# Kernel optimization log

Measured on AMD Instinct MI355X. Metric: run time of the kernel, lower is better.

Reference implementation:

```python
import jax, jax.numpy as jnp
import numpy as np

DIM = 128
HEADS = 4
GH, GW = 14, 14
N = GH * GW            # 196
POS_DIM = (DIM // 4) // 4  # 8, per DynamicPosBias(dim//4): pos_dim = (dim//4)//4
B_ = 1024
NW = 64
EPS = 1e-5


def _make_bias_tables():
    # biases: all relative (dh, dw) offsets, shape ((2*GH-1)*(2*GW-1), 2)
    h = np.arange(1 - GH, GH)
    w = np.arange(1 - GW, GW)
    bh, bw = np.meshgrid(h, w, indexing='ij')
    biases = np.stack([bh.ravel(), bw.ravel()], axis=1).astype(np.float32)
    # relative_position_index: (N, N) int
    ch, cw = np.meshgrid(np.arange(GH), np.arange(GW), indexing='ij')
    coords = np.stack([ch.ravel(), cw.ravel()])          # (2, N)
    rel = coords[:, :, None] - coords[:, None, :]        # (2, N, N)
    rel = rel.transpose(1, 2, 0).copy()
    rel[:, :, 0] += GH - 1
    rel[:, :, 1] += GW - 1
    rel[:, :, 0] *= 2 * GW - 1
    idx = rel.sum(-1).astype(np.int32)                   # (N, N)
    return jnp.asarray(biases), jnp.asarray(idx)


def setup_inputs() -> dict:
    key = jax.random.key(0)
    ks = jax.random.split(key, 12)
    s_in = 1.0 / np.sqrt(DIM)
    s_p = 1.0 / np.sqrt(POS_DIM)
    biases, rel_idx = _make_bias_tables()
    return {
        'x': jax.random.normal(ks[0], (B_, N, DIM), jnp.float32),
        'mask': jnp.zeros((NW, N, N), jnp.float32),
        # qkv / proj (stored as (in, out), i.e. torch weight transposed)
        'qkv_w': jax.random.normal(ks[1], (DIM, 3 * DIM), jnp.float32) * s_in,
        'qkv_b': jnp.zeros((3 * DIM,), jnp.float32),
        'proj_w': jax.random.normal(ks[2], (DIM, DIM), jnp.float32) * s_in,
        'proj_b': jnp.zeros((DIM,), jnp.float32),
        # DynamicPosBias params
        'pos_proj_w': jax.random.normal(ks[3], (2, POS_DIM), jnp.float32) * 0.5,
        'pos_proj_b': jnp.zeros((POS_DIM,), jnp.float32),
        'ln1_w': jnp.ones((POS_DIM,), jnp.float32), 'ln1_b': jnp.zeros((POS_DIM,), jnp.float32),
        'fc1_w': jax.random.normal(ks[4], (POS_DIM, POS_DIM), jnp.float32) * s_p,
        'fc1_b': jnp.zeros((POS_DIM,), jnp.float32),
        'ln2_w': jnp.ones((POS_DIM,), jnp.float32), 'ln2_b': jnp.zeros((POS_DIM,), jnp.float32),
        'fc2_w': jax.random.normal(ks[5], (POS_DIM, POS_DIM), jnp.float32) * s_p,
        'fc2_b': jnp.zeros((POS_DIM,), jnp.float32),
        'ln3_w': jnp.ones((POS_DIM,), jnp.float32), 'ln3_b': jnp.zeros((POS_DIM,), jnp.float32),
        'fc3_w': jax.random.normal(ks[6], (POS_DIM, HEADS), jnp.float32) * s_p,
        'fc3_b': jnp.zeros((HEADS,), jnp.float32),
        'biases': biases,       # ((2GH-1)*(2GW-1), 2) float32
        'rel_idx': rel_idx,     # (N, N) int32
    }


def _ln(x, w, b):
    mu = x.mean(-1, keepdims=True)
    var = ((x - mu) ** 2).mean(-1, keepdims=True)
    return (x - mu) * jax.lax.rsqrt(var + EPS) * w + b


def reference(x, mask, qkv_w, qkv_b, proj_w, proj_b,
              pos_proj_w, pos_proj_b,
              ln1_w, ln1_b, fc1_w, fc1_b,
              ln2_w, ln2_b, fc2_w, fc2_b,
              ln3_w, ln3_b, fc3_w, fc3_b,
              biases, rel_idx):
    B, n, C = x.shape
    hd = C // HEADS
    scale = hd ** -0.5

    qkv = (x @ qkv_w + qkv_b).reshape(B, n, 3, HEADS, hd)
    q, k, v = jnp.moveaxis(qkv, 2, 0)          # each (B, n, H, hd)
    q = q * scale
    attn = jnp.einsum('bqhd,bkhd->bhqk', q, k)  # (B, H, n, n)

    # DynamicPosBias (residual=False): pos3(pos2(pos1(pos_proj(biases))))
    p = biases @ pos_proj_w + pos_proj_b
    p = jax.nn.relu(_ln(p, ln1_w, ln1_b)) @ fc1_w + fc1_b
    p = jax.nn.relu(_ln(p, ln2_w, ln2_b)) @ fc2_w + fc2_b
    p = jax.nn.relu(_ln(p, ln3_w, ln3_b)) @ fc3_w + fc3_b   # (L, H)
    rpb = p[rel_idx]                            # (n, n, H) gather
    attn = attn + jnp.transpose(rpb, (2, 0, 1))[None]

    nW = mask.shape[0]
    attn = attn.reshape(B // nW, nW, HEADS, n, n) + mask[None, :, None]
    attn = jax.nn.softmax(attn.reshape(B, HEADS, n, n), axis=-1)

    out = jnp.einsum('bhqk,bkhd->bqhd', attn, v).reshape(B, n, C)
    return out @ proj_w + proj_b
```

## Files before the change

kernel.cpp:

```cpp
#include <hip/hip_runtime.h>
#include <stdint.h>

#define N_TOK 196
#define DIM   128
#define HEADS 4
#define NWIN  64
#define SCALE 0.17677669529663687f
#define PS_LD 232

typedef __bf16 bf16x8 __attribute__((ext_vector_type(8)));
typedef float  f32x4  __attribute__((ext_vector_type(4)));

__device__ __forceinline__ unsigned short f2bf(float f) {
  unsigned r;
  asm("v_cvt_pk_bf16_f32 %0, %1, %2" : "=v"(r) : "v"(f), "v"(f));
  return (unsigned short)r;
}
__device__ __forceinline__ unsigned pack2(float a, float b) {
  unsigned r;
  asm("v_cvt_pk_bf16_f32 %0, %1, %2" : "=v"(r) : "v"(a), "v"(b));
  return r;
}

__global__ void prep_kernel(
    const float* __restrict__ qkv_w, const float* __restrict__ proj_w,
    const float* __restrict__ biases,
    const float* __restrict__ pos_proj_w, const float* __restrict__ pos_proj_b,
    const float* __restrict__ ln1_w, const float* __restrict__ ln1_b,
    const float* __restrict__ fc1_w, const float* __restrict__ fc1_b,
    const float* __restrict__ ln2_w, const float* __restrict__ ln2_b,
    const float* __restrict__ fc2_w, const float* __restrict__ fc2_b,
    const float* __restrict__ ln3_w, const float* __restrict__ ln3_b,
    const float* __restrict__ fc3_w, const float* __restrict__ fc3_b,
    unsigned short* __restrict__ wqkv_t, unsigned short* __restrict__ wproj_t,
    float* __restrict__ ptab)
{
  const int tid = threadIdx.x, blk = blockIdx.x;
  if (blk < 3) {
    int r = blk * 256 + tid;
    if (r < 729) {
      float v[8], t[8];
      float b0 = biases[2*r], b1 = biases[2*r+1];
      for (int j = 0; j < 8; ++j)
        v[j] = b0 * pos_proj_w[j] + b1 * pos_proj_w[8+j] + pos_proj_b[j];
      const float* lws[3] = {ln1_w, ln2_w, ln3_w};
      const float* lbs[3] = {ln1_b, ln2_b, ln3_b};
      const float* fws[3] = {fc1_w, fc2_w, fc3_w};
      const float* fbs[3] = {fc1_b, fc2_b, fc3_b};
      for (int L = 0; L < 3; ++L) {
        float mu = 0.f;  for (int j=0;j<8;++j) mu += v[j];  mu *= 0.125f;
        float var = 0.f; for (int j=0;j<8;++j){ float d=v[j]-mu; var+=d*d; } var *= 0.125f;
        float rs = rsqrtf(var + 1e-5f);
        for (int j=0;j<8;++j){ float u=(v[j]-mu)*rs*lws[L][j]+lbs[L][j]; t[j]=fmaxf(u,0.f); }
        int nout = (L==2) ? 4 : 8;
        for (int o=0;o<nout;++o){ float s=fbs[L][o]; for (int j=0;j<8;++j) s += t[j]*fws[L][j*nout+o]; v[o]=s; }
      }
      for (int hh=0; hh<4; ++hh) ptab[r*4+hh] = v[hh];
    }
  } else if (blk < 7) {
    for (int i = (blk-3)*256 + tid; i < 384*128; i += 1024) {
      int col = i >> 7, k = i & 127;
      wqkv_t[i] = f2bf(qkv_w[k*384 + col]);
    }
  } else {
    for (int i = tid; i < 128*128; i += 256) {
      int col = i >> 7, k = i & 127;
      wproj_t[i] = f2bf(proj_w[k*128 + col]);
    }
  }
}

__global__ void comb_kernel(const int* __restrict__ rel_idx,
                            const float* __restrict__ ptab,
                            const float* __restrict__ mask,
                            float* __restrict__ combT)
{
  int blk = blockIdx.x;
  int w = blk / 196, k = blk - w*196;
  int q = threadIdx.x;
  if (q < N_TOK) {
    int idx = rel_idx[q*N_TOK + k];
    float mv = mask[((size_t)w*N_TOK + q)*N_TOK + k];
    #pragma unroll
    for (int h = 0; h < 4; ++h)
      combT[((size_t)(w*4 + h)*196 + k)*196 + q] = ptab[idx*4 + h] + mv;
  }
}

__launch_bounds__(256, 2)
__global__ void qkv_kernel(const float* __restrict__ x,
                           const float* __restrict__ qkv_b,
                           const unsigned short* __restrict__ wqkv_t,
                           unsigned short* __restrict__ q_g,
                           unsigned short* __restrict__ k_g,
                           unsigned short* __restrict__ vt_g)
{
  const int tid = threadIdx.x;
  const int wave = tid >> 6, lane = tid & 63, lr = lane & 15, lg = lane >> 4;
  const int b = blockIdx.x;
  const float* xb = x + (size_t)b * (N_TOK*DIM);

  bf16x8 wf[6][4];
  float  bq[6];
  f32x4  bv[6];
  #pragma unroll
  for (int i = 0; i < 6; ++i) {
    const int g = wave*6 + i;
    #pragma unroll
    for (int kc = 0; kc < 4; ++kc)
      wf[i][kc] = *(const bf16x8*)(wqkv_t + (g*16 + lr)*128 + kc*32 + lg*8);
    if (g < 16) {
      bq[i] = qkv_b[g*16 + lr];
      bv[i] = (f32x4){0.f,0.f,0.f,0.f};
    } else {
      bq[i] = 0.f;
      #pragma unroll
      for (int r = 0; r < 4; ++r) bv[i][r] = qkv_b[g*16 + lg*4 + r];
    }
  }

  auto load_xf = [&](int rt, bf16x8* xf) {
    const int arow = rt*16 + lr;
    #pragma unroll
    for (int kc = 0; kc < 4; ++kc) {
      union { unsigned u[4]; bf16x8 v; } c;
      if (arow < N_TOK) {
        float4 p0 = *(const float4*)(xb + arow*DIM + kc*32 + lg*8);
        float4 p1 = *(const float4*)(xb + arow*DIM + kc*32 + lg*8 + 4);
        c.u[0] = pack2(p0.x, p0.y); c.u[1] = pack2(p0.z, p0.w);
        c.u[2] = pack2(p1.x, p1.y); c.u[3] = pack2(p1.z, p1.w);
      } else {
        c.u[0] = c.u[1] = c.u[2] = c.u[3] = 0u;
      }
      xf[kc] = c.v;
    }
  };

  bf16x8 xf[4], xfn[4];
  load_xf(0, xf);
  for (int rt = 0; rt < 13; ++rt) {
    if (rt < 12) load_xf(rt + 1, xfn);
    #pragma unroll
    for (int i = 0; i < 6; ++i) {
      const int g = wave*6 + i;
      f32x4 acc = {0.f,0.f,0.f,0.f};
      if (g >= 16) {
        #pragma unroll
        for (int kc = 0; kc < 4; ++kc)
          acc = __builtin_amdgcn_mfma_f32_16x16x32_bf16(wf[i][kc], xf[kc], acc, 0, 0, 0);
        const int dt = g - 16;
        #pragma unroll
        for (int r = 0; r < 4; ++r)
          vt_g[((size_t)b*128 + dt*16 + lg*4 + r)*224 + rt*16 + lr] =
              f2bf(acc[r] + bv[i][r]);
      } else {
        #pragma unroll
        for (int kc = 0; kc < 4; ++kc)
          acc = __builtin_amdgcn_mfma_f32_16x16x32_bf16(xf[kc], wf[i][kc], acc, 0, 0, 0);
        const int cs = (g < 8) ? g*16 : (g-8)*16;
        unsigned short* dst = (g < 8) ? q_g : k_g;
        const float mul = (g < 8) ? SCALE : 1.f;
        #pragma unroll
        for (int r = 0; r < 4; ++r)
          dst[((size_t)(b*4 + (cs>>5))*208 + rt*16 + lg*4 + r)*32 + (cs&31) + lr] =
              f2bf((acc[r] + bq[i]) * mul);
      }
    }
    #pragma unroll
    for (int kc = 0; kc < 4; ++kc) xf[kc] = xfn[kc];
  }
}

__launch_bounds__(256, 3)
__global__ void attn_kernel(const unsigned short* __restrict__ q_g,
                            const unsigned short* __restrict__ k_g,
                            const unsigned short* __restrict__ vt_g,
                            const float* __restrict__ combT,
                            float* __restrict__ out)
{
  __shared__ unsigned short psw_all[4*16*PS_LD];
  const int tid = threadIdx.x;
  const int wave = tid >> 6, lane = tid & 63, lr = lane & 15, lg = lane >> 4;
  const int wgt = blockIdx.x;
  const int v  = (wgt & 7)*512 + (wgt >> 3);
  const int bi = v & 15, wh = v >> 4;
  const int b  = bi*64 + (wh >> 2), h = wh & 3;
  const int bh = b*4 + h;
  unsigned short* psw = psw_all + wave*(16*PS_LD);

  for (int i = lane; i < 256; i += 64)
    psw[(i >> 4)*PS_LD + 208 + (i & 15)] = 0;

  const unsigned short* qb = q_g + (size_t)bh*(208*32);
  const unsigned short* kb = k_g + (size_t)bh*(208*32);
  const unsigned short* vb = vt_g + (size_t)bh*(32*224);
  const float* cbase = combT + (size_t)wh*(196*196);

  bf16x8 kfr[13];
  #pragma unroll
  for (int kt = 0; kt < 13; ++kt)
    kfr[kt] = *(const bf16x8*)(kb + (kt*16 + lr)*32 + lg*8);

  for (int qt = wave; qt < 13; qt += 4) {
    bf16x8 aq = *(const bf16x8*)(qb + (qt*16 + lr)*32 + lg*8);

    f32x4 s[13];
    __builtin_amdgcn_s_setprio(1);
    #pragma unroll
    for (int kt = 0; kt < 13; ++kt) {
      f32x4 z = {0.f,0.f,0.f,0.f};
      s[kt] = __builtin_amdgcn_mfma_f32_16x16x32_bf16(aq, kfr[kt], z, 0, 0, 0);
    }
    __builtin_amdgcn_s_setprio(0);

    #pragma unroll
    for (int kt = 0; kt < 13; ++kt) {
      int c = kt*16 + lr;
      if (c < N_TOK)
        s[kt] += *(const f32x4*)(cbase + (size_t)c*196 + qt*16 + lg*4);
    }
    if (lr >= 4) s[12] = (f32x4){-1e30f,-1e30f,-1e30f,-1e30f};

    float linv[4];
    #pragma unroll
    for (int r = 0; r < 4; ++r) {
      float m = s[0][r];
      #pragma unroll
      for (int kt = 1; kt < 13; ++kt) m = fmaxf(m, s[kt][r]);
      #pragma unroll
      for (int off = 1; off < 16; off <<= 1) m = fmaxf(m, __shfl_xor(m, off));
      float ssum = 0.f;
      #pragma unroll
      for (int kt = 0; kt < 13; ++kt) {
        float p = __expf(s[kt][r] - m);
        s[kt][r] = p; ssum += p;
      }
      #pragma unroll
      for (int off = 1; off < 16; off <<= 1) ssum += __shfl_xor(ssum, off);
      linv[r] = 1.f / ssum;
    }
    #pragma unroll
    for (int r = 0; r < 4; ++r) {
      int prow = lg*4 + r;
      #pragma unroll
      for (int kt = 0; kt < 13; ++kt)
        psw[prow*PS_LD + kt*16 + lr] = f2bf(s[kt][r]);
    }
    asm volatile("s_waitcnt lgkmcnt(0)" ::: "memory");
    __builtin_amdgcn_s_setprio(1);
    #pragma unroll
    for (int c2 = 0; c2 < 2; ++c2) {
      f32x4 o = {0.f,0.f,0.f,0.f};
      #pragma unroll
      for (int kc = 0; kc < 7; ++kc) {
        bf16x8 ap = *(const bf16x8*)(psw + lr*PS_LD + kc*32 + lg*8);
        bf16x8 bv = *(const bf16x8*)(vb + (c2*16 + lr)*224 + kc*32 + lg*8);
        o = __builtin_amdgcn_mfma_f32_16x16x32_bf16(ap, bv, o, 0, 0, 0);
      }
      #pragma unroll
      for (int r = 0; r < 4; ++r) {
        int row = qt*16 + lg*4 + r;
        if (row < N_TOK)
          out[((size_t)b*N_TOK + row)*DIM + h*32 + c2*16 + lr] = o[r] * linv[r];
      }
    }
    __builtin_amdgcn_s_setprio(0);
  }
}

__launch_bounds__(256, 4)
__global__ void proj_kernel(float* __restrict__ out,
                            const unsigned short* __restrict__ wproj_t,
                            const float* __restrict__ proj_b)
{
  __shared__ unsigned short aos[64*136];
  const int tid = threadIdx.x;
  const int wave = tid >> 6, lane = tid & 63, lr = lane & 15, lg = lane >> 4;
  const size_t row0 = (size_t)blockIdx.x * 64;
  const float* src = out + row0*DIM;

  bf16x8 wf[2][4];
  float bias[2];
  #pragma unroll
  for (int i = 0; i < 2; ++i) {
    int ct = wave*2 + i;
    bias[i] = proj_b[ct*16 + lr];
    #pragma unroll
    for (int kc = 0; kc < 4; ++kc)
      wf[i][kc] = *(const bf16x8*)(wproj_t + (ct*16 + lr)*128 + kc*32 + lg*8);
  }

  for (int i = tid; i < 64*32; i += 256) {
    int lrow = i >> 5, c4 = i & 31;
    float4 v = ((const float4*)src)[i];
    ((uint2*)aos)[lrow*34 + c4] = make_uint2(pack2(v.x, v.y), pack2(v.z, v.w));
  }
  __syncthreads();

  for (int rt = 0; rt < 4; ++rt) {
    bf16x8 af[4];
    #pragma unroll
    for (int kc = 0; kc < 4; ++kc)
      af[kc] = *(const bf16x8*)(aos + (rt*16 + lr)*136 + kc*32 + lg*8);
    #pragma unroll
    for (int i = 0; i < 2; ++i) {
      f32x4 acc = {0.f,0.f,0.f,0.f};
      #pragma unroll
      for (int kc = 0; kc < 4; ++kc)
        acc = __builtin_amdgcn_mfma_f32_16x16x32_bf16(af[kc], wf[i][kc], acc, 0, 0, 0);
      #pragma unroll
      for (int r = 0; r < 4; ++r) {
        size_t grow = row0 + rt*16 + lg*4 + r;
        out[grow*DIM + (wave*2 + i)*16 + lr] = acc[r] + bias[i];
      }
    }
  }
}

extern "C" void kernel_launch(void* const* d_in, const int* in_sizes, int n_in,
                              void* d_out, int out_size, void* d_ws, size_t ws_size,
                              hipStream_t stream)
{
  const float* x          = (const float*)d_in[0];
  const float* mask       = (const float*)d_in[1];
  const float* qkv_w      = (const float*)d_in[2];
  const float* qkv_b      = (const float*)d_in[3];
  const float* proj_w     = (const float*)d_in[4];
  const float* proj_b     = (const float*)d_in[5];
  const float* pos_proj_w = (const float*)d_in[6];
  const float* pos_proj_b = (const float*)d_in[7];
  const float* ln1_w = (const float*)d_in[8];
  const float* ln1_b = (const float*)d_in[9];
  const float* fc1_w = (const float*)d_in[10];
  const float* fc1_b = (const float*)d_in[11];
  const float* ln2_w = (const float*)d_in[12];
  const float* ln2_b = (const float*)d_in[13];
  const float* fc2_w = (const float*)d_in[14];
  const float* fc2_b = (const float*)d_in[15];
  const float* ln3_w = (const float*)d_in[16];
  const float* ln3_b = (const float*)d_in[17];
  const float* fc3_w = (const float*)d_in[18];
  const float* fc3_b = (const float*)d_in[19];
  const float* biases = (const float*)d_in[20];
  const int*   rel_idx = (const int*)d_in[21];

  char* ws = (char*)d_ws;
  unsigned short* wqkv_t  = (unsigned short*)(ws);
  unsigned short* wproj_t = (unsigned short*)(ws + 98304);
  float*          ptab    = (float*)(ws + 131072);
  float*          combT   = (float*)(ws + 147456);
  unsigned short* q_g     = (unsigned short*)(ws + 39485696);
  unsigned short* k_g     = (unsigned short*)(ws + 94011648);
  unsigned short* vt_g    = (unsigned short*)(ws + 148537600);
  float* out = (float*)d_out;

  prep_kernel<<<8, 256, 0, stream>>>(qkv_w, proj_w, biases, pos_proj_w, pos_proj_b,
      ln1_w, ln1_b, fc1_w, fc1_b, ln2_w, ln2_b, fc2_w, fc2_b,
      ln3_w, ln3_b, fc3_w, fc3_b, wqkv_t, wproj_t, ptab);
  comb_kernel<<<NWIN*N_TOK, 256, 0, stream>>>(rel_idx, ptab, mask, combT);
  qkv_kernel<<<1024, 256, 0, stream>>>(x, qkv_b, wqkv_t, q_g, k_g, vt_g);
  attn_kernel<<<1024*HEADS, 256, 0, stream>>>(q_g, k_g, vt_g, combT, out);
  proj_kernel<<<(1024*N_TOK)/64, 256, 0, stream>>>(out, wproj_t, proj_b);
}
```

Measured before the change: 415.5 us.

## Split attention into single-wave blocks per query chunk with XCD-aware mapping

The attention kernel now launches one 64-thread block per (batch, head, query-chunk), giving 16384 blocks instead of 4096 four-wave blocks. Blocks are mapped so each XCD handles a contiguous set of window/head combos, which keeps the bias table in that XCD's L2. The combined bias loads are also hoisted ahead of the QK MFMAs so their latency can overlap with compute. Each block reloads the full K fragments, so K traffic rises fourfold, and the uneven 4/3/3/3 chunk split leaves some load imbalance.

```diff
diff --git a/kernel.cpp b/kernel.cpp
--- a/kernel.cpp
+++ b/kernel.cpp
@@ -171,22 +171,25 @@
   }
 }
 
-__launch_bounds__(256, 3)
+__launch_bounds__(64, 4)
 __global__ void attn_kernel(const unsigned short* __restrict__ q_g,
                             const unsigned short* __restrict__ k_g,
                             const unsigned short* __restrict__ vt_g,
                             const float* __restrict__ combT,
                             float* __restrict__ out)
 {
-  __shared__ unsigned short psw_all[4*16*PS_LD];
-  const int tid = threadIdx.x;
-  const int wave = tid >> 6, lane = tid & 63, lr = lane & 15, lg = lane >> 4;
-  const int wgt = blockIdx.x;
-  const int v  = (wgt & 7)*512 + (wgt >> 3);
-  const int bi = v & 15, wh = v >> 4;
-  const int b  = bi*64 + (wh >> 2), h = wh & 3;
-  const int bh = b*4 + h;
-  unsigned short* psw = psw_all + wave*(16*PS_LD);
+  __shared__ unsigned short psw[16*PS_LD];
+  const int lane = threadIdx.x, lr = lane & 15, lg = lane >> 4;
+  const int id = blockIdx.x;
+  const int xcd = id & 7, slot = id >> 3;
+  const int whl = slot >> 6, rem = slot & 63;
+  const int wh  = xcd*32 + whl;
+  const int b   = (rem >> 2)*64 + (wh >> 2);
+  const int h   = wh & 3;
+  const int qc  = rem & 3;
+  const int bh  = b*4 + h;
+  const int qt0 = (qc == 0) ? 0 : 1 + qc*3;
+  const int nqt = (qc == 0) ? 4 : 3;
 
   for (int i = lane; i < 256; i += 64)
     psw[(i >> 4)*PS_LD + 208 + (i & 15)] = 0;
@@ -201,8 +204,17 @@
   for (int kt = 0; kt < 13; ++kt)
     kfr[kt] = *(const bf16x8*)(kb + (kt*16 + lr)*32 + lg*8);
 
-  for (int qt = wave; qt < 13; qt += 4) {
+  for (int qi = 0; qi < nqt; ++qi) {
+    const int qt = qt0 + qi;
     bf16x8 aq = *(const bf16x8*)(qb + (qt*16 + lr)*32 + lg*8);
+
+    f32x4 cmb[13];
+    #pragma unroll
+    for (int kt = 0; kt < 13; ++kt) {
+      int c = kt*16 + lr;
+      cmb[kt] = (c < N_TOK) ? *(const f32x4*)(cbase + (size_t)c*196 + qt*16 + lg*4)
+                            : (f32x4){0.f,0.f,0.f,0.f};
+    }
 
     f32x4 s[13];
     __builtin_amdgcn_s_setprio(1);
@@ -214,11 +226,7 @@
     __builtin_amdgcn_s_setprio(0);
 
     #pragma unroll
-    for (int kt = 0; kt < 13; ++kt) {
-      int c = kt*16 + lr;
-      if (c < N_TOK)
-        s[kt] += *(const f32x4*)(cbase + (size_t)c*196 + qt*16 + lg*4);
-    }
+    for (int kt = 0; kt < 13; ++kt) s[kt] += cmb[kt];
     if (lr >= 4) s[12] = (f32x4){-1e30f,-1e30f,-1e30f,-1e30f};
 
     float linv[4];
@@ -359,6 +367,6 @@
       ln3_w, ln3_b, fc3_w, fc3_b, wqkv_t, wproj_t, ptab);
   comb_kernel<<<NWIN*N_TOK, 256, 0, stream>>>(rel_idx, ptab, mask, combT);
   qkv_kernel<<<1024, 256, 0, stream>>>(x, qkv_b, wqkv_t, q_g, k_g, vt_g);
-  attn_kernel<<<1024*HEADS, 256, 0, stream>>>(q_g, k_g, vt_g, combT, out);
+  attn_kernel<<<16384, 64, 0, stream>>>(q_g, k_g, vt_g, combT, out);
   proj_kernel<<<(1024*N_TOK)/64, 256, 0, stream>>>(out, wproj_t, proj_b);
 }
```

After: 572.6 us. 1.38x slower.
